# Kernel tuning notes

Measured on AMD Instinct MI355X. Metric: run time of the kernel, lower is better.

The kernel has to match this reference:

```python
import jax, jax.numpy as jnp
import numpy as np

C = 100000
D = 512
KEEP_RATIO = 0.5
EPS = 1.1920929e-07  # torch.finfo(float32).eps
K = max(1, int(C * KEEP_RATIO))


def _l2norm(x):
    # F.normalize(dim=-1): x / max(||x||, eps)
    n = jnp.linalg.norm(x, axis=-1, keepdims=True)
    return x / jnp.maximum(n, EPS)


def setup_inputs() -> dict:
    key = jax.random.key(0)
    k1, k2, k3 = jax.random.split(key, 3)
    tensor = jax.random.normal(k1, (1024, D), dtype=jnp.float32)
    target = jax.random.randint(k2, (1024,), 0, C, dtype=jnp.int32)
    # xavier_normal_ on (C, D): std = sqrt(2 / (C + D))
    std = np.sqrt(2.0 / (C + D)).astype(np.float32)
    weight = jax.random.normal(k3, (C, D), dtype=jnp.float32) * std
    return {"tensor": tensor, "target": target, "weight": weight}


def reference(tensor, target, weight):
    # --- target mining (no-grad in original) ---
    t_n = _l2norm(tensor)            # (B, D)
    w_n = _l2norm(weight)            # (C, D)
    # max over batch of cosine similarity -> per-class score (C,)
    scores = jnp.max(jnp.einsum("bd,cd->bc", t_n, w_n), axis=0)
    # ground-truth classes always kept
    scores = scores.at[target].set(2.0)
    _, topk_idx = jax.lax.top_k(scores, K)
    subsample = jnp.sort(topk_idx)                       # (K,) ascending
    # remap targets into subsampled index space (targets guaranteed present)
    new_target = jnp.searchsorted(subsample, target).astype(jnp.int32)
    # --- head ---
    w_sub = weight[subsample]                            # (K, D) gather
    logits = jnp.einsum("bd,kd->bk", _l2norm(tensor), _l2norm(w_sub))
    return logits, new_target
```

## Files before the change

### kernel.cpp

```cpp
#include <hip/hip_runtime.h>

#define C_CLS 100000
#define D_DIM 512
#define B_ROWS 1024
#define K_KEEP 50000
#define EPS_F 1.1920929e-07f
#define MB_CT 64
#define BAND 2e-3f
#define DELTA 4e-4f
#define RMAX 32768

typedef short v8s __attribute__((ext_vector_type(8)));
typedef float v4f __attribute__((ext_vector_type(4)));

struct Ctrl { unsigned prefix; unsigned need; };

__device__ __forceinline__ unsigned key_of(float f){
  unsigned u = __float_as_uint(f);
  return (u & 0x80000000u) ? ~u : (u | 0x80000000u);
}
__device__ __forceinline__ float key_inv(unsigned k){
  unsigned u = (k & 0x80000000u) ? (k & 0x7FFFFFFFu) : ~k;
  return __uint_as_float(u);
}
__device__ __forceinline__ unsigned short f2bf_rne(float f){
  unsigned u = __float_as_uint(f);
  unsigned r = (u + 0x7FFFu + ((u >> 16) & 1u)) >> 16;
  return (unsigned short)r;
}
__device__ __forceinline__ float bf2f(unsigned short h){
  return __uint_as_float(((unsigned)h) << 16);
}


__global__ __launch_bounds__(64) void norm_t_kernel(const float* __restrict__ t, float* __restrict__ tn,
                                                    unsigned short* __restrict__ tnph, unsigned short* __restrict__ tnpl,
                                                    const int* __restrict__ tgt, unsigned* __restrict__ keys){
  int row = blockIdx.x, lane = threadIdx.x;
  if (lane == 0) atomicMax(&keys[tgt[row]], key_of(2.0f));
  const float4* p = (const float4*)(t + (size_t)row * D_DIM);
  float4 a = p[lane*2+0], b = p[lane*2+1];
  float s = a.x*a.x + a.y*a.y + a.z*a.z + a.w*a.w
          + b.x*b.x + b.y*b.y + b.z*b.z + b.w*b.w;
  #pragma unroll
  for (int off = 32; off; off >>= 1) s += __shfl_xor(s, off);
  float den = fmaxf(sqrtf(s), EPS_F);
  float o[8] = {a.x/den, a.y/den, a.z/den, a.w/den, b.x/den, b.y/den, b.z/den, b.w/den};
  float4* q = (float4*)(tn + (size_t)row * D_DIM);
  q[lane*2+0] = make_float4(o[0],o[1],o[2],o[3]);
  q[lane*2+1] = make_float4(o[4],o[5],o[6],o[7]);
  v8s hv, lv;
  #pragma unroll
  for (int j = 0; j < 8; ++j){
    unsigned short h = f2bf_rne(o[j]);
    hv[j] = (short)h;
    lv[j] = (short)f2bf_rne(o[j] - bf2f(h));
  }
  size_t di = (size_t)((row & ~15) + (lane >> 2)) * 512 + (lane & 3) * 128 + (row & 15) * 8;
  *(v8s*)(tnph + di) = hv;
  *(v8s*)(tnpl + di) = lv;
}

__device__ __forceinline__ void load_a2(const unsigned short* __restrict__ tp, int b0, int ks, int lane, v8s* dst){
  #pragma unroll
  for (int i = 0; i < 2; ++i){
    int t = b0 + i*16 + (ks >> 5);
    dst[i] = *(const v8s*)(tp + (size_t)t * 512 + lane * 8);
  }
}

__global__ __launch_bounds__(512, 4) void mine_kernel(
    const unsigned short* __restrict__ tnph, const unsigned short* __restrict__ tnpl,
    const float* __restrict__ w, unsigned* __restrict__ keys,
    float* __restrict__ S, float* __restrict__ winv_g){
  __shared__ unsigned short lw[MB_CT * D_DIM];
  __shared__ float wn[MB_CT];
  const int tid = threadIdx.x;
  const int lane = tid & 63;
  const int cb = blockIdx.x * MB_CT;
  #pragma unroll
  for (int st = 0; st < 8; ++st){
    int g = tid + st * 512;
    int row = g >> 6, fc = g & 63;
    int c = cb + row; if (c >= C_CLS) c = C_CLS - 1;
    const float4* src = (const float4*)(w + (size_t)c * D_DIM + fc * 8);
    float4 v0 = src[0], v1 = src[1];
    float vv[8] = {v0.x,v0.y,v0.z,v0.w,v1.x,v1.y,v1.z,v1.w};
    float s = 0.f;
    #pragma unroll
    for (int j = 0; j < 8; ++j) s += vv[j]*vv[j];
    #pragma unroll
    for (int off = 32; off; off >>= 1) s += __shfl_xor(s, off);
    if (lane == 0) wn[row] = 1.0f / fmaxf(sqrtf(s), EPS_F);
    v8s hv;
    #pragma unroll
    for (int j = 0; j < 8; ++j) hv[j] = (short)f2bf_rne(vv[j]);
    int t = (row >> 4) * 16 + (fc >> 2);
    int kslot = fc & 3;
    int m = ((fc >> 2) & 1) * 4 + kslot;
    int a16 = t * 64 + kslot * 16 + ((row & 15) ^ m);
    *(v8s*)&lw[(size_t)a16 * 8] = hv;
  }
  __syncthreads();
  if (tid < MB_CT && cb + tid < C_CLS) winv_g[cb + tid] = wn[tid];

  const int wv = tid >> 6;
  const int lr = lane & 15, lg = lane >> 4;
  const int bbase = wv * 128;
  float runmax[4] = {-1e30f,-1e30f,-1e30f,-1e30f};
  v4f acc[4][2];
  #pragma unroll
  for (int j = 0; j < 4; ++j)
    #pragma unroll
    for (int i = 0; i < 2; ++i) acc[j][i] = (v4f){0.f,0.f,0.f,0.f};

  v8s cah[2], cal[2];
  load_a2(tnph, bbase, 0, lane, cah);
  load_a2(tnpl, bbase, 0, lane, cal);

  for (int it = 0; it < 64; ++it){
    const int chunk = it >> 4, kt = it & 15;
    const int b0 = bbase + chunk * 32;
    v8s nah[2], nal[2];
    if (it < 63){
      int nit = it + 1;
      int nb0 = bbase + (nit >> 4) * 32, nks = (nit & 15) << 5;
      load_a2(tnph, nb0, nks, lane, nah);
      load_a2(tnpl, nb0, nks, lane, nal);
    }
    v8s bh[4];
    {
      int m = (kt & 1) * 4 + lg;
      int ci = (lr ^ m);
      #pragma unroll
      for (int j = 0; j < 4; ++j){
        int t = j * 16 + kt;
        int a16 = t * 64 + lg * 16 + ci;
        bh[j] = *(const v8s*)&lw[(size_t)a16 * 8];
      }
    }
    #pragma unroll
    for (int j = 0; j < 4; ++j)
      #pragma unroll
      for (int i = 0; i < 2; ++i){
        acc[j][i] = __builtin_amdgcn_mfma_f32_16x16x32_bf16(cah[i], bh[j], acc[j][i], 0, 0, 0);
        acc[j][i] = __builtin_amdgcn_mfma_f32_16x16x32_bf16(cal[i], bh[j], acc[j][i], 0, 0, 0);
      }
    if ((it & 15) == 15){
      #pragma unroll
      for (int j = 0; j < 4; ++j){
        float mm = acc[j][0][0];
        #pragma unroll
        for (int i = 0; i < 2; ++i)
          #pragma unroll
          for (int r = 0; r < 4; ++r) mm = fmaxf(mm, acc[j][i][r]);
        runmax[j] = fmaxf(runmax[j], mm);
        int cls = cb + j*16 + lr;
        if (cls < C_CLS){
          size_t tb = ((size_t)((cb >> 4) + j) * 32 + (b0 >> 5)) * 512;
          #pragma unroll
          for (int i = 0; i < 2; ++i){
            float4 v = make_float4(acc[j][i][0], acc[j][i][1], acc[j][i][2], acc[j][i][3]);
            *(float4*)(S + tb + i * 256 + lane * 4) = v;
          }
        }
        #pragma unroll
        for (int i = 0; i < 2; ++i) acc[j][i] = (v4f){0.f,0.f,0.f,0.f};
      }
    }
    if (it < 63){
      #pragma unroll
      for (int i = 0; i < 2; ++i){ cah[i] = nah[i]; cal[i] = nal[i]; }
    }
  }
  #pragma unroll
  for (int j = 0; j < 4; ++j){
    float m = runmax[j];
    m = fmaxf(m, __shfl_xor(m, 16));
    m = fmaxf(m, __shfl_xor(m, 32));
    int cls = cb + j*16 + lr;
    if (lg == 0 && cls < C_CLS)
      atomicMax(&keys[cls], key_of(m * wn[j*16 + lr]));
  }
}

__global__ __launch_bounds__(256) void histsel_kernel(const unsigned* __restrict__ keys, unsigned* __restrict__ hist,
                                                      unsigned* __restrict__ done, Ctrl* __restrict__ ctrl, int shift){
  __shared__ unsigned h[256];
  __shared__ int lastf;
  int t = threadIdx.x;
  h[t] = 0u;
  __syncthreads();
  unsigned himask = (shift >= 24) ? 0u : (0xFFFFFFFFu << (shift + 8));
  unsigned prefix = (shift == 24) ? 0u : (ctrl->prefix & himask);
  for (int c = blockIdx.x * 256 + t; c < C_CLS; c += gridDim.x * 256){
    unsigned k = keys[c];
    if ((k & himask) == prefix) atomicAdd(&h[(k >> shift) & 255], 1u);
  }
  __syncthreads();
  if (h[t]) atomicAdd(&hist[t], h[t]);
  __threadfence();
  if (t == 0) lastf = (atomicAdd(done, 1u) == (unsigned)(gridDim.x - 1));
  __syncthreads();
  if (lastf){
    unsigned v = __hip_atomic_load(&hist[t], __ATOMIC_RELAXED, __HIP_MEMORY_SCOPE_AGENT);
    h[t] = v;
    __syncthreads();
    if (t == 0){
      unsigned need = (shift == 24) ? (unsigned)K_KEEP : ctrl->need;
      unsigned pfx  = (shift == 24) ? 0u : ctrl->prefix;
      unsigned cum = 0; int b;
      for (b = 255; b >= 0; --b){
        if (cum + h[b] >= need) break;
        cum += h[b];
      }
      if (b < 0) b = 0;
      ctrl->prefix = pfx | ((unsigned)b << shift);
      ctrl->need = need - cum;
      __hip_atomic_store(done, 0u, __ATOMIC_RELAXED, __HIP_MEMORY_SCOPE_AGENT);
    }
    __hip_atomic_store(&hist[t], 0u, __ATOMIC_RELAXED, __HIP_MEMORY_SCOPE_AGENT);
  }
}

__global__ void band_kernel(const unsigned* __restrict__ keys, const Ctrl* __restrict__ ctrl,
                            int* __restrict__ rlist, int* __restrict__ rcount){
  int c = blockIdx.x * 256 + threadIdx.x;
  if (c >= C_CLS) return;
  unsigned k = keys[c];
  if (k == key_of(2.0f)) return;
  float t = key_inv(ctrl->prefix);
  if (fabsf(key_inv(k) - t) <= BAND){
    int i = atomicAdd(rcount, 1);
    if (i < RMAX) rlist[i] = c;
  }
}

__global__ __launch_bounds__(256) void refine_kernel(
    const float* __restrict__ tn, const float* __restrict__ w,
    const float* __restrict__ winv, const float* __restrict__ S,
    const int* __restrict__ rlist, const int* __restrict__ rcount,
    unsigned* __restrict__ keys){
  __shared__ float red[256];
  __shared__ double dred[256];
  __shared__ int cand[32];
  __shared__ int ncand;
  int n = *rcount; if (n > RMAX) n = RMAX;
  int t = threadIdx.x;
  for (int i = blockIdx.x; i < n; i += gridDim.x){
    int c = rlist[i];
    const int ct = c >> 4, lr = c & 15;
    size_t sa = ((size_t)(ct * 32 + (t >> 3)) << 9) + (((t >> 2) & 1) << 8) + (((t & 3) * 16 + lr) << 2);
    v4f sv = *(const v4f*)(S + sa);
    float m = fmaxf(fmaxf(sv[0],sv[1]), fmaxf(sv[2],sv[3]));
    red[t] = m; __syncthreads();
    for (int off2 = 128; off2; off2 >>= 1){
      if (t < off2) red[t] = fmaxf(red[t], red[t+off2]);
      __syncthreads();
    }
    float thr = red[0] - DELTA;
    if (t == 0) ncand = 0;
    __syncthreads();
    #pragma unroll
    for (int e = 0; e < 4; ++e){
      if (sv[e] >= thr){
        int ci = atomicAdd(&ncand, 1);
        if (ci < 32) cand[ci] = t*4 + e;
      }
    }
    __syncthreads();
    int nc = ncand; if (nc > 32) nc = 32;
    const float* wrow = w + (size_t)c * D_DIM;
    double w0 = (double)wrow[2*t], w1 = (double)wrow[2*t+1];
    double best = -1e300;
    for (int q = 0; q < nc; ++q){
      int b = cand[q];
      const float* tr = tn + (size_t)b * D_DIM;
      double p = fma((double)tr[2*t], w0, (double)tr[2*t+1] * w1);
      dred[t] = p; __syncthreads();
      for (int off2 = 128; off2; off2 >>= 1){
        if (t < off2) dred[t] += dred[t+off2];
        __syncthreads();
      }
      if (t == 0) best = fmax(best, dred[0]);
      __syncthreads();
    }
    if (t == 0) keys[c] = key_of((float)(best * (double)winv[c]));
    __syncthreads();
  }
}

__global__ __launch_bounds__(256) void scanA_kernel(const unsigned* __restrict__ keys, const Ctrl* __restrict__ ctrl,
                                                    uint2* __restrict__ bsum2, unsigned* __restrict__ done2, int nb){
  __shared__ unsigned red[256];
  __shared__ int lastf;
  int t = threadIdx.x;
  unsigned T = ctrl->prefix;
  int base = blockIdx.x * 1024 + t * 4;
  unsigned pack = 0;
  #pragma unroll
  for (int j = 0; j < 4; ++j){
    int c = base + j;
    if (c < C_CLS){
      unsigned k = keys[c];
      if (k > T) pack += 0x10000u;
      else if (k == T) pack += 1u;
    }
  }
  red[t] = pack; __syncthreads();
  for (int off = 128; off; off >>= 1){
    if (t < off) red[t] += red[t + off];
    __syncthreads();
  }
  if (t == 0) bsum2[blockIdx.x] = make_uint2(red[0] >> 16, red[0] & 0xFFFFu);
  __threadfence();
  if (t == 0) lastf = (atomicAdd(done2, 1u) == (unsigned)(gridDim.x - 1));
  __syncthreads();
  if (lastf && t == 0){
    unsigned rg = 0, re = 0;
    for (int i = 0; i < nb; ++i){
      unsigned vx = __hip_atomic_load(&bsum2[i].x, __ATOMIC_RELAXED, __HIP_MEMORY_SCOPE_AGENT);
      unsigned vy = __hip_atomic_load(&bsum2[i].y, __ATOMIC_RELAXED, __HIP_MEMORY_SCOPE_AGENT);
      __hip_atomic_store(&bsum2[i].x, rg, __ATOMIC_RELAXED, __HIP_MEMORY_SCOPE_AGENT);
      __hip_atomic_store(&bsum2[i].y, re, __ATOMIC_RELAXED, __HIP_MEMORY_SCOPE_AGENT);
      rg += vx; re += vy;
    }
    __hip_atomic_store(done2, 0u, __ATOMIC_RELAXED, __HIP_MEMORY_SCOPE_AGENT);
  }
}

__global__ __launch_bounds__(256) void scanC_kernel(const unsigned* __restrict__ keys, const Ctrl* __restrict__ ctrl,
                                                    const uint2* __restrict__ bsum2, unsigned* __restrict__ pos,
                                                    int* __restrict__ sel){
  __shared__ unsigned ls[256];
  int t = threadIdx.x;
  unsigned T = ctrl->prefix, need = ctrl->need;
  int base = blockIdx.x * 1024 + t * 4;
  unsigned gtv[4], eqv[4], pack = 0;
  #pragma unroll
  for (int j = 0; j < 4; ++j){
    int c = base + j;
    unsigned k = (c < C_CLS) ? keys[c] : 0u;
    gtv[j] = (c < C_CLS && k > T) ? 1u : 0u;
    eqv[j] = (c < C_CLS && k == T) ? 1u : 0u;
    pack += (gtv[j] << 16) + eqv[j];
  }
  ls[t] = pack; __syncthreads();
  for (int off = 1; off < 256; off <<= 1){
    unsigned v = (t >= off) ? ls[t - off] : 0u;
    __syncthreads();
    ls[t] += v;
    __syncthreads();
  }
  unsigned excl = ls[t] - pack;
  uint2 bs = bsum2[blockIdx.x];
  unsigned gtx = bs.x + (excl >> 16);
  unsigned eqx = bs.y + (excl & 0xFFFFu);
  #pragma unroll
  for (int j = 0; j < 4; ++j){
    int c = base + j;
    if (c < C_CLS){
      unsigned p = gtx + (eqx < need ? eqx : need);
      pos[c] = p;
      if (gtv[j] || (eqv[j] && eqx < need)) sel[p] = c;
      gtx += gtv[j]; eqx += eqv[j];
    }
  }
}

__global__ void ntgt_kernel(const int* __restrict__ tgt, const unsigned* __restrict__ pos, float* __restrict__ out){
  int b = blockIdx.x * 256 + threadIdx.x;
  if (b < B_ROWS) out[(size_t)B_ROWS * K_KEEP + b] = (float)pos[tgt[b]];
}

__global__ __launch_bounds__(256) void head_copy_kernel(const float* __restrict__ S, const float* __restrict__ winv,
                                                        const int* __restrict__ sel, float* __restrict__ out){
  __shared__ float tl[64][68];
  __shared__ float wsc[64];
  int k0 = blockIdx.y * 64;
  int b0 = blockIdx.x * 64;
  int tid = threadIdx.x;
  int nk = K_KEEP - k0; if (nk > 64) nk = 64;
  if (tid < 64){
    int kk = k0 + tid;
    wsc[tid] = (kk < K_KEEP) ? winv[sel[kk]] : 0.f;
  }
  int r = tid >> 4, lq = tid & 15;
  #pragma unroll
  for (int itr = 0; itr < 4; ++itr){
    int i = itr * 16 + r;
    if (i < nk){
      int c = sel[k0 + i];
      int ct = c >> 4, clr = c & 15;
      size_t sa = ((size_t)(ct * 32 + (b0 >> 5) + (lq >> 3)) << 9)
                + (((lq >> 2) & 1) << 8) + (((lq & 3) * 16 + clr) << 2);
      float4 v = *(const float4*)(S + sa);
      *(float4*)&tl[i][lq * 4] = v;
    }
  }
  __syncthreads();
  #pragma unroll
  for (int itw = 0; itw < 4; ++itw){
    int bb = itw * 16 + r;
    int kk = lq * 4;
    size_t obase = (size_t)(b0 + bb) * K_KEEP + k0;
    if (kk + 3 < nk){
      float4 v = make_float4(tl[kk+0][bb]*wsc[kk+0], tl[kk+1][bb]*wsc[kk+1],
                             tl[kk+2][bb]*wsc[kk+2], tl[kk+3][bb]*wsc[kk+3]);
      *(float4*)(out + obase + kk) = v;
    } else {
      for (int e = 0; e < 4; ++e)
        if (kk + e < nk) out[obase + kk + e] = tl[kk+e][bb]*wsc[kk+e];
    }
  }
}

extern "C" void kernel_launch(void* const* d_in, const int* in_sizes, int n_in,
                              void* d_out, int out_size, void* d_ws, size_t ws_size,
                              hipStream_t stream){
  const float* tensor = (const float*)d_in[0];
  const int*   target = (const int*)d_in[1];
  const float* weight = (const float*)d_in[2];
  float* out = (float*)d_out;

  char* ws = (char*)d_ws;
  size_t off = 0;
  auto carve = [&](size_t bytes) -> char* {
    char* p = ws + off;
    off = (off + bytes + 511) & ~(size_t)511;
    return p;
  };
  float*          tn   = (float*)carve((size_t)B_ROWS * D_DIM * 4);
  unsigned short* tnph = (unsigned short*)carve((size_t)B_ROWS * D_DIM * 2);
  unsigned short* tnpl = (unsigned short*)carve((size_t)B_ROWS * D_DIM * 2);
  float*          winv = (float*)carve((size_t)C_CLS * 4);
  size_t zs = off;
  unsigned* keys   = (unsigned*)carve((size_t)C_CLS * 4);
  unsigned* hist   = (unsigned*)carve(256 * 4);
  unsigned* done   = (unsigned*)carve(64);
  unsigned* done2  = (unsigned*)carve(64);
  int*      rcount = (int*)carve(64);
  size_t ze = off;
  Ctrl*     ctrl   = (Ctrl*)carve(64);
  uint2*    bsum2  = (uint2*)carve(128 * 8);
  int*      rlist  = (int*)carve((size_t)RMAX * 4);
  unsigned* pos    = (unsigned*)carve((size_t)C_CLS * 4);
  int*      sel    = (int*)carve((size_t)K_KEEP * 4);
  float*    S      = (float*)carve((size_t)(C_CLS + 64) * B_ROWS * 4);
  (void)in_sizes; (void)n_in; (void)out_size; (void)ws_size;

  hipMemsetAsync(ws + zs, 0, ze - zs, stream);

  norm_t_kernel<<<B_ROWS, 64, 0, stream>>>(tensor, tn, tnph, tnpl, target, keys);

  mine_kernel<<<(C_CLS + MB_CT - 1) / MB_CT, 512, 0, stream>>>(tnph, tnpl, weight, keys, S, winv);

  for (int shift = 24; shift >= 0; shift -= 8)
    histsel_kernel<<<128, 256, 0, stream>>>(keys, hist, done, ctrl, shift);

  band_kernel<<<(C_CLS + 255) / 256, 256, 0, stream>>>(keys, ctrl, rlist, rcount);
  refine_kernel<<<2048, 256, 0, stream>>>(tn, weight, winv, S, rlist, rcount, keys);

  for (int shift = 24; shift >= 0; shift -= 8)
    histsel_kernel<<<128, 256, 0, stream>>>(keys, hist, done, ctrl, shift);

  const int nb = (C_CLS + 1023) / 1024;
  scanA_kernel<<<nb, 256, 0, stream>>>(keys, ctrl, bsum2, done2, nb);
  scanC_kernel<<<nb, 256, 0, stream>>>(keys, ctrl, bsum2, pos, sel);

  ntgt_kernel<<<(B_ROWS + 255) / 256, 256, 0, stream>>>(target, pos, out);
  head_copy_kernel<<<dim3(B_ROWS / 64, (K_KEEP + 63) / 64), 256, 0, stream>>>(S, winv, sel, out);
}
```

Baseline: 657.6 us.

## Iterate head copy over class blocks with coalesced S reads and compaction

The head copy kernel now loops over contiguous blocks of 128 source classes instead of 64 selected output columns. It reads the full S tiles for those classes with coalesced float4 loads and keeps only the selected ones. Each kept class is scattered into a shared tile at its compacted position taken from pos/sel, and contiguous output runs are then written. This replaces scattered gather reads from S with streaming reads, but it reads every class (about twice the needed data) and switches the output writes from float4 to scalar stores.

```diff
diff --git a/kernel.cpp b/kernel.cpp
--- a/kernel.cpp
+++ b/kernel.cpp
@@ -373,45 +373,61 @@
   if (b < B_ROWS) out[(size_t)B_ROWS * K_KEEP + b] = (float)pos[tgt[b]];
 }
 
-__global__ __launch_bounds__(256) void head_copy_kernel(const float* __restrict__ S, const float* __restrict__ winv,
-                                                        const int* __restrict__ sel, float* __restrict__ out){
-  __shared__ float tl[64][68];
-  __shared__ float wsc[64];
-  int k0 = blockIdx.y * 64;
+__global__ __launch_bounds__(256) void head_sel_kernel(const float* __restrict__ S, const float* __restrict__ winv,
+                                                       const int* __restrict__ sel, const unsigned* __restrict__ pos,
+                                                       float* __restrict__ out){
+  __shared__ float tl[64][129];
+  __shared__ float wscl[128];
+  __shared__ short slt[128];
+  __shared__ unsigned ksh[2];
   int b0 = blockIdx.x * 64;
+  int cb = blockIdx.y * 128;
   int tid = threadIdx.x;
-  int nk = K_KEEP - k0; if (nk > 64) nk = 64;
-  if (tid < 64){
-    int kk = k0 + tid;
-    wsc[tid] = (kk < K_KEEP) ? winv[sel[kk]] : 0.f;
-  }
-  int r = tid >> 4, lq = tid & 15;
-  #pragma unroll
-  for (int itr = 0; itr < 4; ++itr){
-    int i = itr * 16 + r;
-    if (i < nk){
-      int c = sel[k0 + i];
-      int ct = c >> 4, clr = c & 15;
-      size_t sa = ((size_t)(ct * 32 + (b0 >> 5) + (lq >> 3)) << 9)
-                + (((lq >> 2) & 1) << 8) + (((lq & 3) * 16 + clr) << 2);
-      float4 v = *(const float4*)(S + sa);
-      *(float4*)&tl[i][lq * 4] = v;
-    }
-  }
-  __syncthreads();
-  #pragma unroll
-  for (int itw = 0; itw < 4; ++itw){
-    int bb = itw * 16 + r;
-    int kk = lq * 4;
-    size_t obase = (size_t)(b0 + bb) * K_KEEP + k0;
-    if (kk + 3 < nk){
-      float4 v = make_float4(tl[kk+0][bb]*wsc[kk+0], tl[kk+1][bb]*wsc[kk+1],
-                             tl[kk+2][bb]*wsc[kk+2], tl[kk+3][bb]*wsc[kk+3]);
-      *(float4*)(out + obase + kk) = v;
-    } else {
-      for (int e = 0; e < 4; ++e)
-        if (kk + e < nk) out[obase + kk + e] = tl[kk+e][bb]*wsc[kk+e];
-    }
+  if (tid == 0) ksh[0] = pos[cb];
+  if (tid == 1) ksh[1] = (cb + 128 < C_CLS) ? pos[cb + 128] : (unsigned)K_KEEP;
+  __syncthreads();
+  unsigned k_start = ksh[0];
+  if (tid < 128){
+    int c = cb + tid;
+    short s = -1;
+    float wv = 0.f;
+    if (c < C_CLS){
+      unsigned p = pos[c];
+      if (p < (unsigned)K_KEEP && sel[p] == c){
+        s = (short)(p - k_start);
+        wv = winv[c];
+      }
+    }
+    slt[tid] = s;
+    wscl[tid] = wv;
+  }
+  __syncthreads();
+  #pragma unroll
+  for (int pass = 0; pass < 8; ++pass){
+    int f = pass * 256 + tid;
+    int g = f >> 7, q = f & 127;
+    int gi = g >> 1, bs = g & 1;
+    size_t tile = ((size_t)((cb >> 4) + gi) * 32) + (b0 >> 5) + bs;
+    float4 v = *(const float4*)(S + tile * 512 + (size_t)q * 4);
+    int cl = gi * 16 + (q & 15);
+    short s = slt[cl];
+    if (s >= 0){
+      int bl = (bs << 5) + (((q >> 6) & 1) << 4) + (((q >> 4) & 3) << 2);
+      float w = wscl[cl];
+      tl[bl+0][s] = v.x * w;
+      tl[bl+1][s] = v.y * w;
+      tl[bl+2][s] = v.z * w;
+      tl[bl+3][s] = v.w * w;
+    }
+  }
+  __syncthreads();
+  int nkk = (int)(ksh[1] - k_start);
+  int wv2 = tid >> 6, lane = tid & 63;
+  for (int rr = 0; rr < 16; ++rr){
+    int b = wv2 * 16 + rr;
+    size_t obase = (size_t)(b0 + b) * K_KEEP + k_start;
+    if (lane < nkk)      out[obase + lane]      = tl[b][lane];
+    if (lane + 64 < nkk) out[obase + lane + 64] = tl[b][lane + 64];
   }
 }
 
@@ -446,7 +462,7 @@
   int*      rlist  = (int*)carve((size_t)RMAX * 4);
   unsigned* pos    = (unsigned*)carve((size_t)C_CLS * 4);
   int*      sel    = (int*)carve((size_t)K_KEEP * 4);
-  float*    S      = (float*)carve((size_t)(C_CLS + 64) * B_ROWS * 4);
+  float*    S      = (float*)carve((size_t)(C_CLS + 128) * B_ROWS * 4);
   (void)in_sizes; (void)n_in; (void)out_size; (void)ws_size;
 
   hipMemsetAsync(ws + zs, 0, ze - zs, stream);
@@ -469,5 +485,5 @@
   scanC_kernel<<<nb, 256, 0, stream>>>(keys, ctrl, bsum2, pos, sel);
 
   ntgt_kernel<<<(B_ROWS + 255) / 256, 256, 0, stream>>>(target, pos, out);
-  head_copy_kernel<<<dim3(B_ROWS / 64, (K_KEEP + 63) / 64), 256, 0, stream>>>(S, winv, sel, out);
-}
+  head_sel_kernel<<<dim3(B_ROWS / 64, (C_CLS + 127) / 128), 256, 0, stream>>>(S, winv, sel, pos, out);
+}
```

Measured after the change: 670.2 us. Within noise of the previous version (+1.9%).

## Recompute head logits with a gathered-weight MFMA GEMM instead of copying from S

Applied to the files above, without the earlier changes.

Replaces the head copy kernel, which gathered per-class columns of the precomputed similarity buffer S, with a new GEMM kernel. It gathers the selected weight rows, converts them to bf16 in LDS, and runs hi/lo split bf16 MFMAs against the normalized tensor, scaling by the inverse weight norm. The aim is to avoid a large scattered read of S in exchange for recomputing about half of the mining GEMM. The mining kernel still writes S, and S's workspace padding shrinks. Output stores become per-element rather than float4, which may reduce write efficiency.

```diff
diff --git a/kernel.cpp b/kernel.cpp
--- a/kernel.cpp
+++ b/kernel.cpp
@@ -181,6 +181,103 @@
     int cls = cb + j*16 + lr;
     if (lg == 0 && cls < C_CLS)
       atomicMax(&keys[cls], key_of(m * wn[j*16 + lr]));
+  }
+}
+
+__global__ __launch_bounds__(512, 4) void head_gemm_kernel(
+    const unsigned short* __restrict__ tnph, const unsigned short* __restrict__ tnpl,
+    const float* __restrict__ w, const float* __restrict__ winv,
+    const int* __restrict__ sel, float* __restrict__ out){
+  __shared__ unsigned short lw[MB_CT * D_DIM];
+  __shared__ float wsc[MB_CT];
+  const int tid = threadIdx.x;
+  const int lane = tid & 63;
+  const int kb = blockIdx.x * MB_CT;
+  #pragma unroll
+  for (int st = 0; st < 8; ++st){
+    int g = tid + st * 512;
+    int row = g >> 6, fc = g & 63;
+    int kidx = kb + row;
+    int c = (kidx < K_KEEP) ? sel[kidx] : sel[0];
+    if (lane == 0) wsc[row] = (kidx < K_KEEP) ? winv[c] : 0.f;
+    const float4* src = (const float4*)(w + (size_t)c * D_DIM + fc * 8);
+    float4 v0 = src[0], v1 = src[1];
+    float vv[8] = {v0.x,v0.y,v0.z,v0.w,v1.x,v1.y,v1.z,v1.w};
+    v8s hv;
+    #pragma unroll
+    for (int j = 0; j < 8; ++j) hv[j] = (short)f2bf_rne(vv[j]);
+    int t = (row >> 4) * 16 + (fc >> 2);
+    int kslot = fc & 3;
+    int m = ((fc >> 2) & 1) * 4 + kslot;
+    int a16 = t * 64 + kslot * 16 + ((row & 15) ^ m);
+    *(v8s*)&lw[(size_t)a16 * 8] = hv;
+  }
+  __syncthreads();
+
+  const int wv = tid >> 6;
+  const int lr = lane & 15, lg = lane >> 4;
+  const int bbase = wv * 128;
+  v4f acc[4][2];
+  #pragma unroll
+  for (int j = 0; j < 4; ++j)
+    #pragma unroll
+    for (int i = 0; i < 2; ++i) acc[j][i] = (v4f){0.f,0.f,0.f,0.f};
+
+  v8s cah[2], cal[2];
+  load_a2(tnph, bbase, 0, lane, cah);
+  load_a2(tnpl, bbase, 0, lane, cal);
+
+  for (int it = 0; it < 64; ++it){
+    const int chunk = it >> 4, kt = it & 15;
+    const int b0 = bbase + chunk * 32;
+    v8s nah[2], nal[2];
+    if (it < 63){
+      int nit = it + 1;
+      int nb0 = bbase + (nit >> 4) * 32, nks = (nit & 15) << 5;
+      load_a2(tnph, nb0, nks, lane, nah);
+      load_a2(tnpl, nb0, nks, lane, nal);
+    }
+    v8s bh[4];
+    {
+      int m = (kt & 1) * 4 + lg;
+      int ci = (lr ^ m);
+      #pragma unroll
+      for (int j = 0; j < 4; ++j){
+        int t = j * 16 + kt;
+        int a16 = t * 64 + lg * 16 + ci;
+        bh[j] = *(const v8s*)&lw[(size_t)a16 * 8];
+      }
+    }
+    #pragma unroll
+    for (int j = 0; j < 4; ++j)
+      #pragma unroll
+      for (int i = 0; i < 2; ++i){
+        acc[j][i] = __builtin_amdgcn_mfma_f32_16x16x32_bf16(cah[i], bh[j], acc[j][i], 0, 0, 0);
+        acc[j][i] = __builtin_amdgcn_mfma_f32_16x16x32_bf16(cal[i], bh[j], acc[j][i], 0, 0, 0);
+      }
+    if ((it & 15) == 15){
+      #pragma unroll
+      for (int j = 0; j < 4; ++j){
+        int k = kb + j*16 + lr;
+        if (k < K_KEEP){
+          float wvv = wsc[j*16 + lr];
+          #pragma unroll
+          for (int i = 0; i < 2; ++i){
+            #pragma unroll
+            for (int r = 0; r < 4; ++r){
+              int b = b0 + i*16 + lg*4 + r;
+              out[(size_t)b * K_KEEP + k] = acc[j][i][r] * wvv;
+            }
+          }
+        }
+        #pragma unroll
+        for (int i = 0; i < 2; ++i) acc[j][i] = (v4f){0.f,0.f,0.f,0.f};
+      }
+    }
+    if (it < 63){
+      #pragma unroll
+      for (int i = 0; i < 2; ++i){ cah[i] = nah[i]; cal[i] = nal[i]; }
+    }
   }
 }
 
@@ -371,48 +468,6 @@
 __global__ void ntgt_kernel(const int* __restrict__ tgt, const unsigned* __restrict__ pos, float* __restrict__ out){
   int b = blockIdx.x * 256 + threadIdx.x;
   if (b < B_ROWS) out[(size_t)B_ROWS * K_KEEP + b] = (float)pos[tgt[b]];
-}
-
-__global__ __launch_bounds__(256) void head_copy_kernel(const float* __restrict__ S, const float* __restrict__ winv,
-                                                        const int* __restrict__ sel, float* __restrict__ out){
-  __shared__ float tl[64][68];
-  __shared__ float wsc[64];
-  int k0 = blockIdx.y * 64;
-  int b0 = blockIdx.x * 64;
-  int tid = threadIdx.x;
-  int nk = K_KEEP - k0; if (nk > 64) nk = 64;
-  if (tid < 64){
-    int kk = k0 + tid;
-    wsc[tid] = (kk < K_KEEP) ? winv[sel[kk]] : 0.f;
-  }
-  int r = tid >> 4, lq = tid & 15;
-  #pragma unroll
-  for (int itr = 0; itr < 4; ++itr){
-    int i = itr * 16 + r;
-    if (i < nk){
-      int c = sel[k0 + i];
-      int ct = c >> 4, clr = c & 15;
-      size_t sa = ((size_t)(ct * 32 + (b0 >> 5) + (lq >> 3)) << 9)
-                + (((lq >> 2) & 1) << 8) + (((lq & 3) * 16 + clr) << 2);
-      float4 v = *(const float4*)(S + sa);
-      *(float4*)&tl[i][lq * 4] = v;
-    }
-  }
-  __syncthreads();
-  #pragma unroll
-  for (int itw = 0; itw < 4; ++itw){
-    int bb = itw * 16 + r;
-    int kk = lq * 4;
-    size_t obase = (size_t)(b0 + bb) * K_KEEP + k0;
-    if (kk + 3 < nk){
-      float4 v = make_float4(tl[kk+0][bb]*wsc[kk+0], tl[kk+1][bb]*wsc[kk+1],
-                             tl[kk+2][bb]*wsc[kk+2], tl[kk+3][bb]*wsc[kk+3]);
-      *(float4*)(out + obase + kk) = v;
-    } else {
-      for (int e = 0; e < 4; ++e)
-        if (kk + e < nk) out[obase + kk + e] = tl[kk+e][bb]*wsc[kk+e];
-    }
-  }
 }
 
 extern "C" void kernel_launch(void* const* d_in, const int* in_sizes, int n_in,
@@ -446,7 +501,7 @@
   int*      rlist  = (int*)carve((size_t)RMAX * 4);
   unsigned* pos    = (unsigned*)carve((size_t)C_CLS * 4);
   int*      sel    = (int*)carve((size_t)K_KEEP * 4);
-  float*    S      = (float*)carve((size_t)(C_CLS + 64) * B_ROWS * 4);
+  float*    S      = (float*)carve((size_t)C_CLS * B_ROWS * 4);
   (void)in_sizes; (void)n_in; (void)out_size; (void)ws_size;
 
   hipMemsetAsync(ws + zs, 0, ze - zs, stream);
@@ -469,5 +524,5 @@
   scanC_kernel<<<nb, 256, 0, stream>>>(keys, ctrl, bsum2, pos, sel);
 
   ntgt_kernel<<<(B_ROWS + 255) / 256, 256, 0, stream>>>(target, pos, out);
-  head_copy_kernel<<<dim3(B_ROWS / 64, (K_KEEP + 63) / 64), 256, 0, stream>>>(S, winv, sel, out);
-}
+  head_gemm_kernel<<<(K_KEEP + MB_CT - 1) / MB_CT, 512, 0, stream>>>(tnph, tnpl, weight, winv, sel, out);
+}
```

New measurement: 697.6 us. 6.1% more time.
